# Kernel optimization log

Measured on AMD Instinct MI355X. Metric: run time of the kernel, lower is better.

Reference implementation:

```python
import jax, jax.numpy as jnp
import numpy as np

WS = (14, 14)
NUM_HEADS = 12
DIM = 768
HEAD_DIM = DIM // NUM_HEADS
N_TOK = WS[0] * WS[1] + 1  # 197 (cls token)
NUM_REL = (2 * WS[0] - 1) * (2 * WS[1] - 1) + 3  # 732
B = 64


def _build_rel_pos_index():
    ch, cw = np.arange(WS[0]), np.arange(WS[1])
    coords = np.stack(np.meshgrid(ch, cw, indexing='ij'))  # [2,h,w]
    cf = coords.reshape(2, -1)  # [2, h*w]
    rel = cf[:, :, None] - cf[:, None, :]  # [2, hw, hw]
    rel = rel.transpose(1, 2, 0).astype(np.int64)
    rel[:, :, 0] += WS[0] - 1
    rel[:, :, 1] += WS[1] - 1
    rel[:, :, 0] *= 2 * WS[1] - 1
    idx = np.zeros((N_TOK, N_TOK), dtype=np.int64)
    idx[1:, 1:] = rel.sum(-1)
    idx[0, 0:] = NUM_REL - 3
    idx[0:, 0] = NUM_REL - 2
    idx[0, 0] = NUM_REL - 1
    return idx.astype(np.int32)


def setup_inputs() -> dict:
    key = jax.random.key(0)
    ks = jax.random.split(key, 7)
    s = 0.02
    return {
        'x': jax.random.normal(ks[0], (B, N_TOK, DIM), jnp.float32),
        'qkv_w': jax.random.normal(ks[1], (3 * DIM, DIM), jnp.float32) * s,
        'q_bias': jax.random.normal(ks[2], (DIM,), jnp.float32) * s,
        'v_bias': jax.random.normal(ks[3], (DIM,), jnp.float32) * s,
        'rpb_table': jax.random.normal(ks[4], (NUM_REL, NUM_HEADS), jnp.float32) * s,
        'proj_w': jax.random.normal(ks[5], (DIM, DIM), jnp.float32) * s,
        'proj_b': jax.random.normal(ks[6], (DIM,), jnp.float32) * s,
        'rel_pos_index': jnp.asarray(_build_rel_pos_index()),
    }


def reference(x, qkv_w, q_bias, v_bias, rpb_table, proj_w, proj_b, rel_pos_index):
    Bb, N, C = x.shape
    scale = HEAD_DIM ** -0.5
    # qkv bias: [q_bias, zeros(k), v_bias]
    qkv_bias = jnp.concatenate([q_bias, jnp.zeros_like(v_bias), v_bias])
    qkv = x @ qkv_w.T + qkv_bias  # [B,N,3C]
    qkv = qkv.reshape(Bb, N, 3, NUM_HEADS, HEAD_DIM).transpose(2, 0, 3, 1, 4)
    q, k, v = qkv[0], qkv[1], qkv[2]  # [B,H,N,hd]
    attn = jnp.einsum('bhnd,bhmd->bhnm', q * scale, k)
    # gather relative position bias: [N,N,H] -> [1,H,N,N]
    rpb = rpb_table[rel_pos_index]  # [N,N,H]
    attn = attn + rpb.transpose(2, 0, 1)[None]
    attn = jax.nn.softmax(attn, axis=-1)
    out = jnp.einsum('bhnm,bhmd->bhnd', attn, v)
    out = out.transpose(0, 2, 1, 3).reshape(Bb, N, NUM_HEADS * HEAD_DIM)
    return out @ proj_w.T + proj_b
```

## Files before the change

kernel.cpp:

```cpp
#include <hip/hip_runtime.h>
#include <hip/hip_bf16.h>
#include <cstdint>
#include <cstddef>

typedef __bf16 bf16x8 __attribute__((ext_vector_type(8)));
typedef float f32x4 __attribute__((ext_vector_type(4)));

#define DI __device__ __forceinline__

DI unsigned short f2bf(float x) {
    union { float f; unsigned int u; } v; v.f = x;
    unsigned int u = v.u;
    u += 0x7FFFu + ((u >> 16) & 1u);
    return (unsigned short)(u >> 16);
}

#define BATCH 64
#define NH 12
#define NTOK 197
#define NTOK_P 208
#define HD 64
#define DIM 768
#define MROWS 12608
#define MPAD 224
#define PLDS 232
#define CPAD 132

DI int xcd_swz(int orig, int nwg) {
    int q = nwg >> 3, r = nwg & 7;
    int x = orig & 7, l = orig >> 3;
    return (x < r ? x * (q + 1) : r * (q + 1) + (x - r) * q) + l;
}


__global__ void cvt_bf16_kernel(const float* __restrict__ in, unsigned short* __restrict__ out, int n4) {
    int i = blockIdx.x * blockDim.x + threadIdx.x;
    if (i >= n4) return;
    float4 f = ((const float4*)in)[i];
    ushort4 o;
    o.x = f2bf(f.x); o.y = f2bf(f.y); o.z = f2bf(f.z); o.w = f2bf(f.w);
    ((ushort4*)out)[i] = o;
}

__global__ void build_rpb_kernel(const float* __restrict__ table, const int* __restrict__ idx,
                                 float* __restrict__ out) {
    int i = blockIdx.x * blockDim.x + threadIdx.x;
    if (i >= NH * NTOK_P * NTOK_P) return;
    int r = i % NTOK_P; int c = (i / NTOK_P) % NTOK_P; int h = i / (NTOK_P * NTOK_P);
    float v = 0.f;
    if (r < NTOK && c < NTOK) v = table[idx[r * NTOK + c] * NH + h];
    out[i] = v;
}

__global__ void zero_vt_pad_kernel(unsigned short* __restrict__ vt) {
    const int npad = MPAD - NTOK;
    int i = blockIdx.x * blockDim.x + threadIdx.x;
    if (i >= BATCH * NH * HD * npad) return;
    int c = NTOK + (i % npad);
    int row = i / npad;
    vt[(size_t)row * MPAD + c] = 0;
}


DI int swz(int row, int col_elem) {
    return (row * 64 + col_elem) ^ ((row & 7) << 3);
}

template<int EPI>
__launch_bounds__(256)
__global__ void gemm_bt_kernel(const unsigned short* __restrict__ A,
                               const unsigned short* __restrict__ W,
                               const float* __restrict__ bias0,
                               const float* __restrict__ bias1,
                               void* __restrict__ out0,
                               unsigned short* __restrict__ out1,
                               unsigned short* __restrict__ out2,
                               int M, int ntiles)
{
    __shared__ __align__(16) unsigned short smem[32768];
    const int K = DIM;
    const int NT = K / 64;
    int wgid = xcd_swz(blockIdx.x, gridDim.x);
    int mt = wgid / ntiles, nt = wgid % ntiles;
    int m0 = mt * 128, n0 = nt * 128;
    int tid = threadIdx.x;
    int lane = tid & 63, w = tid >> 6;
    int wr = (w >> 1) * 64, wc = (w & 1) * 64;

    const int st_row = lane >> 3;
    const int st_col = ((lane & 7) ^ (lane >> 3)) << 3;

    f32x4 acc[4][4] = {};

    auto stage = [&](int buf, int ks) {
        unsigned short* as = smem + buf * 8192;
        unsigned short* bs = smem + 16384 + buf * 8192;
#pragma unroll
        for (int i = 0; i < 4; i++) {
            int s = w * 4 + i;
            int arow = m0 + s * 8 + st_row; if (arow >= M) arow = M - 1;
            __builtin_amdgcn_global_load_lds(
                (const __attribute__((address_space(1))) void*)(A + (size_t)arow * K + ks + st_col),
                (__attribute__((address_space(3))) void*)(as + s * 512), 16, 0, 0);
        }
#pragma unroll
        for (int i = 0; i < 4; i++) {
            int s = w * 4 + i;
            __builtin_amdgcn_global_load_lds(
                (const __attribute__((address_space(1))) void*)(W + (size_t)(n0 + s * 8 + st_row) * K + ks + st_col),
                (__attribute__((address_space(3))) void*)(bs + s * 512), 16, 0, 0);
        }
    };

    stage(0, 0);
    __syncthreads();
    int cur = 0;
    for (int t = 0; t < NT; ++t) {
        if (t + 1 < NT) stage(cur ^ 1, (t + 1) * 64);
        const unsigned short* as = smem + cur * 8192;
        const unsigned short* bs = smem + 16384 + cur * 8192;
#pragma unroll
        for (int kc = 0; kc < 2; kc++) {
            bf16x8 af[4], bfr[4];
#pragma unroll
            for (int x = 0; x < 4; x++)
                af[x] = *(const bf16x8*)&as[swz(wr + x * 16 + (lane & 15), kc * 32 + (lane >> 4) * 8)];
#pragma unroll
            for (int y = 0; y < 4; y++)
                bfr[y] = *(const bf16x8*)&bs[swz(wc + y * 16 + (lane & 15), kc * 32 + (lane >> 4) * 8)];
#pragma unroll
            for (int x = 0; x < 4; x++)
#pragma unroll
                for (int y = 0; y < 4; y++)
                    acc[x][y] = __builtin_amdgcn_mfma_f32_16x16x32_bf16(af[x], bfr[y], acc[x][y], 0, 0, 0);
        }
        __syncthreads();
        cur ^= 1;
    }

    if constexpr (EPI == 1) {
#pragma unroll
        for (int x = 0; x < 4; x++)
#pragma unroll
            for (int y = 0; y < 4; y++)
#pragma unroll
                for (int j = 0; j < 4; j++) {
                    int m = m0 + wr + x * 16 + (lane >> 4) * 4 + j;
                    int n = n0 + wc + y * 16 + (lane & 15);
                    if (m < M)
                        ((float*)out0)[(size_t)m * DIM + n] = acc[x][y][j] + bias0[n];
                }
    } else {
        int which = n0 / DIM;
        int hn0 = n0 - which * DIM;
        unsigned short* lc = smem;

#pragma unroll
        for (int x = 0; x < 4; x++)
#pragma unroll
            for (int y = 0; y < 4; y++)
#pragma unroll
                for (int j = 0; j < 4; j++) {
                    int ml = wr + x * 16 + (lane >> 4) * 4 + j;
                    int nl = wc + y * 16 + (lane & 15);
                    float val = acc[x][y][j];
                    if (which == 0) val = (val + bias0[hn0 + nl]) * 0.125f;
                    else if (which == 2) val = val + bias1[hn0 + nl];
                    lc[ml * CPAD + nl] = f2bf(val);
                }
        __syncthreads();

        if (which != 2) {
            unsigned short* outq = (which == 0) ? (unsigned short*)out0 : out1;
            int c4 = (lane & 31) * 4;
            int h = (hn0 >> 6) + (c4 >> 6), d = c4 & 63;
            for (int it = 0; it < 16; ++it) {
                int r = it * 8 + w * 2 + (lane >> 5);
                int m = m0 + r;
                if (m >= M) continue;
                int b = m / NTOK, t = m - b * NTOK;
                ushort4 q4 = *(const ushort4*)&lc[r * CPAD + c4];
                *(ushort4*)&outq[(((size_t)b * NH + h) * NTOK_P + t) * HD + d] = q4;
            }
        } else {
            int mh = w >> 1, hs = w & 1;
            int h = (hn0 >> 6) + hs;
            int ml = mh * 64 + lane;
            int m = m0 + ml;
            if (m < M) {
                int b = m / NTOK, t = m - b * NTOK;
                unsigned short* vbase = out2 + (((size_t)b * NH + h) * HD) * MPAD + t;
#pragma unroll 8
                for (int d = 0; d < 64; ++d)
                    vbase[(size_t)d * MPAD] = lc[ml * CPAD + hs * 64 + d];
            }
        }
    }
}


__launch_bounds__(64)
__global__ void attn_kernel(const unsigned short* __restrict__ qbuf,
                            const unsigned short* __restrict__ kbuf,
                            const unsigned short* __restrict__ vt,
                            const float* __restrict__ rpbT,
                            unsigned short* __restrict__ ao)
{
    __shared__ __align__(16) unsigned short p_lds[16][PLDS];
    int bid = xcd_swz(blockIdx.x, gridDim.x);
    int qt = bid % 13, bh = bid / 13;
    int b = bh / NH, h = bh - b * NH;
    int lane = threadIdx.x;
    int r0 = qt * 16;

    {
        int rr = lane >> 2, cc = NTOK_P + (lane & 3) * 4;
        ushort4 z = {0, 0, 0, 0};
        *(ushort4*)&p_lds[rr][cc] = z;
    }

    const size_t kqbase = (size_t)bh * NTOK_P * HD;
    int qrow = r0 + (lane & 15);
    bf16x8 qf0 = *(const bf16x8*)&qbuf[kqbase + (size_t)qrow * HD + (lane >> 4) * 8];
    bf16x8 qf1 = *(const bf16x8*)&qbuf[kqbase + (size_t)qrow * HD + 32 + (lane >> 4) * 8];

    f32x4 s[13];
#pragma unroll
    for (int t = 0; t < 13; t++) {
        int krow = t * 16 + (lane & 15);
        bf16x8 kf0 = *(const bf16x8*)&kbuf[kqbase + (size_t)krow * HD + (lane >> 4) * 8];
        bf16x8 kf1 = *(const bf16x8*)&kbuf[kqbase + (size_t)krow * HD + 32 + (lane >> 4) * 8];
        f32x4 z = {0.f, 0.f, 0.f, 0.f};
        f32x4 a = __builtin_amdgcn_mfma_f32_16x16x32_bf16(qf0, kf0, z, 0, 0, 0);
        s[t] = __builtin_amdgcn_mfma_f32_16x16x32_bf16(qf1, kf1, a, 0, 0, 0);
    }

    int col_l = lane & 15;
    int rbase = r0 + (lane >> 4) * 4;
    float mrow[4] = {-1e30f, -1e30f, -1e30f, -1e30f};
#pragma unroll
    for (int t = 0; t < 13; t++) {
        int col = t * 16 + col_l;
        bool masked = (col >= NTOK);
        float4 rb = *(const float4*)&rpbT[((size_t)h * NTOK_P + col) * NTOK_P + rbase];
        float rbj[4] = {rb.x, rb.y, rb.z, rb.w};
#pragma unroll
        for (int j = 0; j < 4; j++) {
            float v = s[t][j] + rbj[j];
            if (masked) v = -1e30f;
            s[t][j] = v;
            mrow[j] = fmaxf(mrow[j], v);
        }
    }
#pragma unroll
    for (int j = 0; j < 4; j++) {
        float mv = mrow[j];
        mv = fmaxf(mv, __shfl_xor(mv, 1));
        mv = fmaxf(mv, __shfl_xor(mv, 2));
        mv = fmaxf(mv, __shfl_xor(mv, 4));
        mv = fmaxf(mv, __shfl_xor(mv, 8));
        mrow[j] = mv;
    }
    float lrow[4] = {0.f, 0.f, 0.f, 0.f};
#pragma unroll
    for (int t = 0; t < 13; t++)
#pragma unroll
        for (int j = 0; j < 4; j++) {
            float p = __expf(s[t][j] - mrow[j]);
            s[t][j] = p;
            lrow[j] += p;
        }
#pragma unroll
    for (int j = 0; j < 4; j++) {
        float lv = lrow[j];
        lv += __shfl_xor(lv, 1);
        lv += __shfl_xor(lv, 2);
        lv += __shfl_xor(lv, 4);
        lv += __shfl_xor(lv, 8);
        lrow[j] = lv;
    }
#pragma unroll
    for (int t = 0; t < 13; t++)
#pragma unroll
        for (int j = 0; j < 4; j++)
            p_lds[(lane >> 4) * 4 + j][t * 16 + col_l] = f2bf(s[t][j]);

    f32x4 o[4] = {};
    const size_t vbase = (size_t)bh * HD * MPAD;
#pragma unroll
    for (int c = 0; c < 7; c++) {
        bf16x8 pf = *(const bf16x8*)&p_lds[lane & 15][c * 32 + (lane >> 4) * 8];
#pragma unroll
        for (int n = 0; n < 4; n++) {
            bf16x8 vf = *(const bf16x8*)&vt[vbase + (size_t)(n * 16 + (lane & 15)) * MPAD + c * 32 + (lane >> 4) * 8];
            o[n] = __builtin_amdgcn_mfma_f32_16x16x32_bf16(pf, vf, o[n], 0, 0, 0);
        }
    }
#pragma unroll
    for (int n = 0; n < 4; n++)
#pragma unroll
        for (int j = 0; j < 4; j++) {
            int tok = rbase + j;
            if (tok < NTOK) {
                float val = o[n][j] / lrow[j];
                ao[((size_t)b * NTOK + tok) * DIM + h * HD + n * 16 + col_l] = f2bf(val);
            }
        }
}


extern "C" void kernel_launch(void* const* d_in, const int* in_sizes, int n_in,
                              void* d_out, int out_size, void* d_ws, size_t ws_size,
                              hipStream_t stream)
{
    const float* x      = (const float*)d_in[0];
    const float* qkv_w  = (const float*)d_in[1];
    const float* q_bias = (const float*)d_in[2];
    const float* v_bias = (const float*)d_in[3];
    const float* rpb_t  = (const float*)d_in[4];
    const float* proj_w = (const float*)d_in[5];
    const float* proj_b = (const float*)d_in[6];
    const int*   relidx = (const int*)d_in[7];
    float* out = (float*)d_out;

    char* ws = (char*)d_ws;
    const size_t SZ_XBF  = (size_t)MROWS * DIM * 2;
    const size_t SZ_QKVW = (size_t)3 * DIM * DIM * 2;
    const size_t SZ_PRJW = (size_t)DIM * DIM * 2;
    const size_t SZ_QK   = (size_t)BATCH * NH * NTOK_P * HD * 2;
    const size_t SZ_VT   = (size_t)BATCH * NH * HD * MPAD * 2;

    unsigned short* x_bf = (unsigned short*)ws;
    unsigned short* ao   = x_bf;
    size_t off = SZ_XBF;
    unsigned short* qkvw_bf  = (unsigned short*)(ws + off); off += SZ_QKVW;
    unsigned short* projw_bf = (unsigned short*)(ws + off); off += SZ_PRJW;
    unsigned short* qbuf     = (unsigned short*)(ws + off); off += SZ_QK;
    unsigned short* kbuf     = (unsigned short*)(ws + off); off += SZ_QK;
    unsigned short* vtbuf    = (unsigned short*)(ws + off); off += SZ_VT;
    float* rpbf              = (float*)(ws + off);

    cvt_bf16_kernel<<<(MROWS * DIM / 4 + 255) / 256, 256, 0, stream>>>(x, x_bf, MROWS * DIM / 4);
    cvt_bf16_kernel<<<(3 * DIM * DIM / 4 + 255) / 256, 256, 0, stream>>>(qkv_w, qkvw_bf, 3 * DIM * DIM / 4);
    cvt_bf16_kernel<<<(DIM * DIM / 4 + 255) / 256, 256, 0, stream>>>(proj_w, projw_bf, DIM * DIM / 4);
    build_rpb_kernel<<<(NH * NTOK_P * NTOK_P + 255) / 256, 256, 0, stream>>>(rpb_t, relidx, rpbf);
    zero_vt_pad_kernel<<<(BATCH * NH * HD * (MPAD - NTOK) + 255) / 256, 256, 0, stream>>>(vtbuf);

    gemm_bt_kernel<0><<<99 * 18, 256, 0, stream>>>(x_bf, qkvw_bf, q_bias, v_bias,
                                                   (void*)qbuf, kbuf, vtbuf, MROWS, 18);
    attn_kernel<<<BATCH * NH * 13, 64, 0, stream>>>(qbuf, kbuf, vtbuf, rpbf, ao);
    gemm_bt_kernel<1><<<99 * 6, 256, 0, stream>>>(ao, projw_bf, proj_b, nullptr,
                                                  (void*)out, nullptr, nullptr, MROWS, 6);
    (void)in_sizes; (void)n_in; (void)out_size; (void)ws_size;
}
```

Baseline: 207.5 us.

## Deepen GEMM pipeline to 4-stage K=32 buffers with vmcnt-based waits

Restructures the bf16 GEMM main loop from a double-buffered K=64 tile into a four-buffer ring of K=32 tiles with three stages in flight. Each iteration waits on vmcnt counters and uses a single barrier instead of a full __syncthreads. It also adds a new packed, swizzled LDS layout (two rows per 64-element line) and raises wave priority around the MFMA block. The aim is to hide global-to-LDS load latency better and reduce barrier stalls, at the cost of twice as many loop iterations and hand-tuned waitcnt logic that must match the number of loads issued.

```diff
diff --git a/kernel.cpp b/kernel.cpp
--- a/kernel.cpp
+++ b/kernel.cpp
@@ -7,6 +7,8 @@
 typedef float f32x4 __attribute__((ext_vector_type(4)));
 
 #define DI __device__ __forceinline__
+#define AS1 __attribute__((address_space(1)))
+#define AS3 __attribute__((address_space(3)))
 
 DI unsigned short f2bf(float x) {
     union { float f; unsigned int u; } v; v.f = x;
@@ -32,6 +34,12 @@
     return (x < r ? x * (q + 1) : r * (q + 1) + (x - r) * q) + l;
 }
 
+DI int pk(int r, int k) {
+    int prow = r >> 1;
+    int pcol = ((r & 1) << 5) + k;
+    return prow * 64 + (pcol ^ ((prow & 7) << 3));
+}
+
 
 __global__ void cvt_bf16_kernel(const float* __restrict__ in, unsigned short* __restrict__ out, int n4) {
     int i = blockIdx.x * blockDim.x + threadIdx.x;
@@ -61,10 +69,6 @@
     vt[(size_t)row * MPAD + c] = 0;
 }
 
-
-DI int swz(int row, int col_elem) {
-    return (row * 64 + col_elem) ^ ((row & 7) << 3);
-}
 
 template<int EPI>
 __launch_bounds__(256)
@@ -79,63 +83,69 @@
 {
     __shared__ __align__(16) unsigned short smem[32768];
     const int K = DIM;
-    const int NT = K / 64;
+    const int NT = K / 32;
     int wgid = xcd_swz(blockIdx.x, gridDim.x);
     int mt = wgid / ntiles, nt = wgid % ntiles;
     int m0 = mt * 128, n0 = nt * 128;
     int tid = threadIdx.x;
     int lane = tid & 63, w = tid >> 6;
     int wr = (w >> 1) * 64, wc = (w & 1) * 64;
-
-    const int st_row = lane >> 3;
-    const int st_col = ((lane & 7) ^ (lane >> 3)) << 3;
+    int r15 = lane & 15, hi8 = (lane >> 4) * 8;
 
     f32x4 acc[4][4] = {};
 
     auto stage = [&](int buf, int ks) {
-        unsigned short* as = smem + buf * 8192;
-        unsigned short* bs = smem + 16384 + buf * 8192;
-#pragma unroll
-        for (int i = 0; i < 4; i++) {
-            int s = w * 4 + i;
-            int arow = m0 + s * 8 + st_row; if (arow >= M) arow = M - 1;
+        unsigned short* as = smem + buf * 4096;
+        unsigned short* bs = smem + 16384 + buf * 4096;
+#pragma unroll
+        for (int r0 = 0; r0 < 2; ++r0) {
+            int L = r0 * 256 + tid;
+            int prow = L >> 3;
+            int ls = (L & 7) ^ (prow & 7);
+            int rr = (prow << 1) + (ls >> 2);
+            int kk = (ls & 3) << 3;
+            int arow = m0 + rr; if (arow >= M) arow = M - 1;
             __builtin_amdgcn_global_load_lds(
-                (const __attribute__((address_space(1))) void*)(A + (size_t)arow * K + ks + st_col),
-                (__attribute__((address_space(3))) void*)(as + s * 512), 16, 0, 0);
-        }
-#pragma unroll
-        for (int i = 0; i < 4; i++) {
-            int s = w * 4 + i;
+                (const AS1 void*)(A + (size_t)arow * K + ks + kk),
+                (AS3 void*)(as + r0 * 2048 + w * 512), 16, 0, 0);
             __builtin_amdgcn_global_load_lds(
-                (const __attribute__((address_space(1))) void*)(W + (size_t)(n0 + s * 8 + st_row) * K + ks + st_col),
-                (__attribute__((address_space(3))) void*)(bs + s * 512), 16, 0, 0);
+                (const AS1 void*)(W + (size_t)(n0 + rr) * K + ks + kk),
+                (AS3 void*)(bs + r0 * 2048 + w * 512), 16, 0, 0);
         }
     };
 
     stage(0, 0);
-    __syncthreads();
-    int cur = 0;
+    stage(1, 32);
+    stage(2, 64);
+    asm volatile("s_waitcnt vmcnt(8)" ::: "memory");
+    __builtin_amdgcn_sched_barrier(0);
+    __builtin_amdgcn_s_barrier();
+
     for (int t = 0; t < NT; ++t) {
-        if (t + 1 < NT) stage(cur ^ 1, (t + 1) * 64);
-        const unsigned short* as = smem + cur * 8192;
-        const unsigned short* bs = smem + 16384 + cur * 8192;
-#pragma unroll
-        for (int kc = 0; kc < 2; kc++) {
-            bf16x8 af[4], bfr[4];
-#pragma unroll
-            for (int x = 0; x < 4; x++)
-                af[x] = *(const bf16x8*)&as[swz(wr + x * 16 + (lane & 15), kc * 32 + (lane >> 4) * 8)];
+        if (t + 3 < NT) stage((t + 3) & 3, (t + 3) * 32);
+        const unsigned short* as = smem + (t & 3) * 4096;
+        const unsigned short* bs = smem + 16384 + (t & 3) * 4096;
+        bf16x8 af[4], bfr[4];
+#pragma unroll
+        for (int x = 0; x < 4; x++)
+            af[x] = *(const bf16x8*)&as[pk(wr + x * 16 + r15, hi8)];
+#pragma unroll
+        for (int y = 0; y < 4; y++)
+            bfr[y] = *(const bf16x8*)&bs[pk(wc + y * 16 + r15, hi8)];
+        __builtin_amdgcn_s_setprio(1);
+#pragma unroll
+        for (int x = 0; x < 4; x++)
 #pragma unroll
             for (int y = 0; y < 4; y++)
-                bfr[y] = *(const bf16x8*)&bs[swz(wc + y * 16 + (lane & 15), kc * 32 + (lane >> 4) * 8)];
-#pragma unroll
-            for (int x = 0; x < 4; x++)
-#pragma unroll
-                for (int y = 0; y < 4; y++)
-                    acc[x][y] = __builtin_amdgcn_mfma_f32_16x16x32_bf16(af[x], bfr[y], acc[x][y], 0, 0, 0);
-        }
-        __syncthreads();
-        cur ^= 1;
+                acc[x][y] = __builtin_amdgcn_mfma_f32_16x16x32_bf16(af[x], bfr[y], acc[x][y], 0, 0, 0);
+        __builtin_amdgcn_s_setprio(0);
+        asm volatile("s_waitcnt lgkmcnt(0)" ::: "memory");
+        __builtin_amdgcn_sched_barrier(0);
+        if (t < NT - 3)       asm volatile("s_waitcnt vmcnt(8)" ::: "memory");
+        else if (t == NT - 3) asm volatile("s_waitcnt vmcnt(4)" ::: "memory");
+        else                  asm volatile("s_waitcnt vmcnt(0)" ::: "memory");
+        __builtin_amdgcn_sched_barrier(0);
+        __builtin_amdgcn_s_barrier();
     }
 
     if constexpr (EPI == 1) {
@@ -146,7 +156,7 @@
 #pragma unroll
                 for (int j = 0; j < 4; j++) {
                     int m = m0 + wr + x * 16 + (lane >> 4) * 4 + j;
-                    int n = n0 + wc + y * 16 + (lane & 15);
+                    int n = n0 + wc + y * 16 + r15;
                     if (m < M)
                         ((float*)out0)[(size_t)m * DIM + n] = acc[x][y][j] + bias0[n];
                 }
@@ -155,6 +165,7 @@
         int hn0 = n0 - which * DIM;
         unsigned short* lc = smem;
 
+        __syncthreads();
 #pragma unroll
         for (int x = 0; x < 4; x++)
 #pragma unroll
@@ -162,7 +173,7 @@
 #pragma unroll
                 for (int j = 0; j < 4; j++) {
                     int ml = wr + x * 16 + (lane >> 4) * 4 + j;
-                    int nl = wc + y * 16 + (lane & 15);
+                    int nl = wc + y * 16 + r15;
                     float val = acc[x][y][j];
                     if (which == 0) val = (val + bias0[hn0 + nl]) * 0.125f;
                     else if (which == 2) val = val + bias1[hn0 + nl];
```

After: 214.4 us. 1.03x slower.
